# Optimization experiments

Measured on AMD Instinct MI355X. Metric: run time of the kernel, lower is better.

## Reference

```python
import jax, jax.numpy as jnp
import numpy as np

D_MODEL = 1024
NUM_HEADS = 16


def setup_inputs() -> dict:
    key = jax.random.key(0)
    ks = jax.random.split(key, 5)
    std = 1.0 / np.sqrt(D_MODEL)
    def w(k):
        return jnp.clip(jax.random.normal(k, (D_MODEL, D_MODEL), dtype=jnp.float32) * std, -3.0, 3.0)
    return {
        "x": jax.random.normal(ks[0], (4, 2048, D_MODEL), dtype=jnp.float32),
        "Wq": w(ks[1]),
        "Wk": w(ks[2]),
        "Wv": w(ks[3]),
        "Wo": w(ks[4]),
    }


def _mha(x, Wq, Wk, Wv, Wo):
    B, S, D = x.shape
    H = NUM_HEADS
    hd = D // H
    # Linear: y = x @ W.T (weights stored [d_out, d_in])
    def proj(W):
        y = jnp.einsum('bsd,ed->bse', x, W)
        return y.reshape(B, S, H, hd).transpose(0, 2, 1, 3)  # b h s d
    q, k, v = proj(Wq), proj(Wk), proj(Wv)
    scores = jnp.einsum('bhqd,bhkd->bhqk', q, k) / np.sqrt(hd)
    causal = jnp.tril(jnp.ones((S, S), dtype=bool))
    scores = jnp.where(causal, scores, -jnp.inf)
    attn = jax.nn.softmax(scores, axis=-1)
    a = jnp.einsum('bhqk,bhkd->bhqd', attn, v)
    a = a.transpose(0, 2, 1, 3).reshape(B, S, D)
    return jnp.einsum('bsd,ed->bse', a, Wo)


def reference(x, Wq, Wk, Wv, Wo):
    return _mha(x, Wq, Wk, Wv, Wo)
```

## Files before the change

kernel.cpp:

```cpp
#include <hip/hip_runtime.h>
#include <hip/hip_bf16.h>
#include <cstdint>
#include <cstddef>


typedef short bf16x8 __attribute__((ext_vector_type(8)));
typedef float f32x4 __attribute__((ext_vector_type(4)));
typedef unsigned int u32x2 __attribute__((ext_vector_type(2)));

__device__ __forceinline__ short f2bf(float f) {
    union { float f; uint32_t u; } c; c.f = f;
    uint32_t r = c.u + 0x7fffu + ((c.u >> 16) & 1u);
    return (short)(r >> 16);
}

__device__ __forceinline__ unsigned cvt_pk_bf16(float lo, float hi) {
    unsigned r;
    asm("v_cvt_pk_bf16_f32 %0, %1, %2" : "=v"(r) : "v"(lo), "v"(hi));
    return r;
}

#define GLOAD_LDS16(g, l) __builtin_amdgcn_global_load_lds( \
    (const __attribute__((address_space(1))) void*)(g),     \
    (__attribute__((address_space(3))) void*)(l), 16, 0, 0)

__global__ __launch_bounds__(256) void convert_kernel(const float* __restrict__ src,
                                                      short* __restrict__ dst) {
    int i = blockIdx.x * 256 + threadIdx.x;
    const float4* s = (const float4*)src + (size_t)i * 2;
    float4 v0 = s[0], v1 = s[1];
    bf16x8 o;
    o[0] = f2bf(v0.x); o[1] = f2bf(v0.y); o[2] = f2bf(v0.z); o[3] = f2bf(v0.w);
    o[4] = f2bf(v1.x); o[5] = f2bf(v1.y); o[6] = f2bf(v1.z); o[7] = f2bf(v1.w);
    *((bf16x8*)dst + i) = o;
}

__global__ __launch_bounds__(256) void convert_w4(const float* __restrict__ w0,
                                                  const float* __restrict__ w1,
                                                  const float* __restrict__ w2,
                                                  const float* __restrict__ w3,
                                                  short* __restrict__ dst) {
    int id = blockIdx.x;
    const float* s = (id < 512) ? w0 : (id < 1024) ? w1 : (id < 1536) ? w2 : w3;
    int i = (id & 511) * 256 + threadIdx.x;
    const float4* sp = (const float4*)s + (size_t)i * 2;
    float4 v0 = sp[0], v1 = sp[1];
    bf16x8 o;
    o[0] = f2bf(v0.x); o[1] = f2bf(v0.y); o[2] = f2bf(v0.z); o[3] = f2bf(v0.w);
    o[4] = f2bf(v1.x); o[5] = f2bf(v1.y); o[6] = f2bf(v1.z); o[7] = f2bf(v1.w);
    *((bf16x8*)(dst + (size_t)(id >> 9) * 1024 * 1024) + i) = o;
}

template<bool OUT_F32>
__device__ __forceinline__ void gemm_body(const short* __restrict__ A,
                                          const short* __restrict__ Bw,
                                          void* __restrict__ Outp,
                                          float escale) {
    __shared__ short As[128 * 32];
    __shared__ short Bs[128 * 32];
    const int tid = threadIdx.x;
    const int lane = tid & 63, w = tid >> 6;
    const int wr = w >> 1, wc = w & 1;
    const int l15 = lane & 15, l4 = lane >> 4;
    const int lin = blockIdx.y * 8 + blockIdx.x;
    const int eff = (lin & 7) * 64 + (lin >> 3);
    const size_t m0 = (size_t)(eff >> 3) * 128;
    const size_t n0 = (size_t)(eff & 7) * 128;

    f32x4 acc[4][4];
    const f32x4 zf = {0.f, 0.f, 0.f, 0.f};
    #pragma unroll
    for (int i = 0; i < 4; i++)
        #pragma unroll
        for (int j = 0; j < 4; j++) acc[i][j] = zf;

    for (int k0 = 0; k0 < 1024; k0 += 32) {
        #pragma unroll
        for (int r = 0; r < 2; r++) {
            int c = r * 256 + tid;
            int row = c >> 2, q = c & 3;
            GLOAD_LDS16(A  + (m0 + row) * 1024 + k0 + q * 8, &As[(r * 256 + w * 64) * 8]);
            GLOAD_LDS16(Bw + (n0 + row) * 1024 + k0 + q * 8, &Bs[(r * 256 + w * 64) * 8]);
        }
        __syncthreads();

        bf16x8 af[4], bfr[4];
        #pragma unroll
        for (int mi = 0; mi < 4; mi++)
            af[mi] = *(const bf16x8*)&As[(wr * 64 + mi * 16 + l15) * 32 + l4 * 8];
        #pragma unroll
        for (int ni = 0; ni < 4; ni++)
            bfr[ni] = *(const bf16x8*)&Bs[(wc * 64 + ni * 16 + l15) * 32 + l4 * 8];
        #pragma unroll
        for (int mi = 0; mi < 4; mi++)
            #pragma unroll
            for (int ni = 0; ni < 4; ni++)
                acc[mi][ni] = __builtin_amdgcn_mfma_f32_16x16x32_bf16(af[mi], bfr[ni], acc[mi][ni], 0, 0, 0);
        __syncthreads();
    }

    #pragma unroll
    for (int mi = 0; mi < 4; mi++) {
        #pragma unroll
        for (int ni = 0; ni < 4; ni++) {
            size_t row = m0 + wr * 64 + mi * 16 + (l4 << 2);
            size_t col = n0 + wc * 64 + ni * 16 + l15;
            #pragma unroll
            for (int j = 0; j < 4; j++) {
                float v = acc[mi][ni][j] * escale;
                if (OUT_F32) ((float*)Outp)[(row + j) * 1024 + col] = v;
                else         ((short*)Outp)[(row + j) * 1024 + col] = f2bf(v);
            }
        }
    }
}

__global__ __launch_bounds__(256) void gemm_qkv(const short* __restrict__ xb,
                                                const short* __restrict__ Wq,
                                                const short* __restrict__ Wk,
                                                const short* __restrict__ Wv,
                                                short* __restrict__ Q,
                                                short* __restrict__ K,
                                                short* __restrict__ V) {
    const short* Bw = (blockIdx.z == 0) ? Wq : (blockIdx.z == 1) ? Wk : Wv;
    short* Out      = (blockIdx.z == 0) ? Q  : (blockIdx.z == 1) ? K  : V;
    float sc = (blockIdx.z == 0) ? 0.18033688011112042f : 1.0f;
    gemm_body<false>(xb, Bw, Out, sc);
}

__global__ __launch_bounds__(256) void gemm_out(const short* __restrict__ Aw,
                                                const short* __restrict__ Wo,
                                                float* __restrict__ Out) {
    gemm_body<true>(Aw, Wo, Out, 1.0f);
}

__global__ __launch_bounds__(256) void transpose_v(const short* __restrict__ Vw,
                                                   short* __restrict__ Vt) {
    __shared__ short T[64][72];
    const int tid = threadIdx.x;
    const int s0 = blockIdx.x * 64;
    const int bh = blockIdx.y, b = bh >> 4, h = bh & 15;
    const int r = tid >> 2, c = tid & 3;
    const size_t srow = (size_t)(b * 2048 + s0 + r) * 1024 + h * 64 + c * 16;
    *(bf16x8*)&T[r][c * 16]     = *(const bf16x8*)&Vw[srow];
    *(bf16x8*)&T[r][c * 16 + 8] = *(const bf16x8*)&Vw[srow + 8];
    __syncthreads();
    short tmp[16];
    #pragma unroll
    for (int i = 0; i < 16; i++) tmp[i] = T[c * 16 + i][r];
    bf16x8 o0, o1;
    #pragma unroll
    for (int i = 0; i < 8; i++) { o0[i] = tmp[i]; o1[i] = tmp[8 + i]; }
    size_t orow = (size_t)(bh * 64 + r) * 2048 + s0 + c * 16;
    *(bf16x8*)&Vt[orow] = o0;
    *(bf16x8*)&Vt[orow + 8] = o1;
}

__global__ __launch_bounds__(512, 4) void attn_kernel(const short* __restrict__ Q,
                                                      const short* __restrict__ K,
                                                      const short* __restrict__ Vt,
                                                      short* __restrict__ Aout) {
    __shared__ __align__(16) short K_lds[2][64 * 64];
    __shared__ __align__(16) short V_lds[2][64 * 64];
    __shared__ __align__(16) short P_lds[8][16][72];
    const int tid = threadIdx.x;
    const int lane = tid & 63, w = tid >> 6;
    const int l15 = lane & 15, l4 = lane >> 4;
    const int bh = blockIdx.x, b = bh >> 4, h = bh & 15;
    const int y = blockIdx.y;
    const int qblk = (y < 4) ? (7 - y) : (y - 4);
    const int qw0 = qblk * 256 + w * 32;
    const short* Qg = Q + (size_t)b * 2048 * 1024 + h * 64;
    const short* Kg = K + (size_t)b * 2048 * 1024 + h * 64;
    const short* Vg = Vt + (size_t)bh * 64 * 2048;

    const int srow = (lane >> 3);
    const int scol = ((lane & 7) ^ srow) * 8;

    bf16x8 qfr[2][2];
    #pragma unroll
    for (int qf = 0; qf < 2; qf++)
        #pragma unroll
        for (int ks = 0; ks < 2; ks++)
            qfr[qf][ks] = *(const bf16x8*)&Qg[(size_t)(qw0 + qf * 16 + l15) * 1024 + ks * 32 + l4 * 8];

    const f32x4 zf = {0.f, 0.f, 0.f, 0.f};
    f32x4 oacc[4][2];
    float l_s[2] = {0.f, 0.f};
    #pragma unroll
    for (int df = 0; df < 4; df++)
        #pragma unroll
        for (int qf = 0; qf < 2; qf++) oacc[df][qf] = zf;

    const int lim = 4 * qblk + 3;

#define KV_RD(base, r, cb) (*(const bf16x8*)((const char*)(base) + (r) * 128 + ((cb) ^ (((r) & 7) << 4))))

    GLOAD_LDS16(Kg + (size_t)(w * 8 + srow) * 1024 + scol, &K_lds[0][w * 512]);
    GLOAD_LDS16(Vg + (size_t)(w * 8 + srow) * 2048 + scol, &V_lds[0][w * 512]);
    __syncthreads();

    int buf = 0;
    for (int t = 0; t <= lim; ++t) {
        const int kv0 = t * 64;
        if (t < lim) {
            const int nv0 = kv0 + 64;
            GLOAD_LDS16(Kg + (size_t)(nv0 + w * 8 + srow) * 1024 + scol, &K_lds[buf ^ 1][w * 512]);
            GLOAD_LDS16(Vg + (size_t)(w * 8 + srow) * 2048 + nv0 + scol, &V_lds[buf ^ 1][w * 512]);
        }

        const int lim_w = (qw0 + 31) >> 6;
        if (t <= lim_w) {
            const short* Kb = K_lds[buf];
            const short* Vb = V_lds[buf];

            f32x4 sacc[4][2];
            #pragma unroll
            for (int kvf = 0; kvf < 4; kvf++)
                #pragma unroll
                for (int qf = 0; qf < 2; qf++) sacc[kvf][qf] = zf;
            __builtin_amdgcn_s_setprio(1);
            #pragma unroll
            for (int kvf = 0; kvf < 4; kvf++) {
                bf16x8 kf0 = KV_RD(Kb, kvf * 16 + l15, l4 * 16);
                bf16x8 kf1 = KV_RD(Kb, kvf * 16 + l15, 64 + l4 * 16);
                #pragma unroll
                for (int qf = 0; qf < 2; qf++) {
                    sacc[kvf][qf] = __builtin_amdgcn_mfma_f32_16x16x32_bf16(kf0, qfr[qf][0], sacc[kvf][qf], 0, 0, 0);
                    sacc[kvf][qf] = __builtin_amdgcn_mfma_f32_16x16x32_bf16(kf1, qfr[qf][1], sacc[kvf][qf], 0, 0, 0);
                }
            }
            __builtin_amdgcn_s_setprio(0);

            if (t == lim_w) {
                #pragma unroll
                for (int kvf = 0; kvf < 4; kvf++)
                    #pragma unroll
                    for (int qf = 0; qf < 2; qf++)
                        #pragma unroll
                        for (int j = 0; j < 4; j++) {
                            int kvg = kv0 + kvf * 16 + l4 * 4 + j;
                            int qg  = qw0 + qf * 16 + l15;
                            if (kvg > qg) sacc[kvf][qf][j] = -1e30f;
                        }
            }

            #pragma unroll
            for (int qf = 0; qf < 2; qf++) {
                float rk[4];
                #pragma unroll
                for (int kvf = 0; kvf < 4; kvf++) {
                    float p0 = __builtin_amdgcn_exp2f(sacc[kvf][qf][0]);
                    float p1 = __builtin_amdgcn_exp2f(sacc[kvf][qf][1]);
                    float p2 = __builtin_amdgcn_exp2f(sacc[kvf][qf][2]);
                    float p3 = __builtin_amdgcn_exp2f(sacc[kvf][qf][3]);
                    sacc[kvf][qf][0] = p0; sacc[kvf][qf][1] = p1;
                    sacc[kvf][qf][2] = p2; sacc[kvf][qf][3] = p3;
                    rk[kvf] = (p0 + p1) + (p2 + p3);
                }
                l_s[qf] += (rk[0] + rk[1]) + (rk[2] + rk[3]);
                #pragma unroll
                for (int kvf = 0; kvf < 4; kvf++) {
                    u32x2 pr;
                    pr[0] = cvt_pk_bf16(sacc[kvf][qf][0], sacc[kvf][qf][1]);
                    pr[1] = cvt_pk_bf16(sacc[kvf][qf][2], sacc[kvf][qf][3]);
                    *(u32x2*)&P_lds[w][l15][kvf * 16 + l4 * 4] = pr;
                }
                asm volatile("s_waitcnt lgkmcnt(0)" ::: "memory");
                __builtin_amdgcn_sched_barrier(0);

                bf16x8 pf0 = *(const bf16x8*)&P_lds[w][l15][l4 * 8];
                bf16x8 pf1 = *(const bf16x8*)&P_lds[w][l15][32 + l4 * 8];

                __builtin_amdgcn_s_setprio(1);
                #pragma unroll
                for (int df = 0; df < 4; df++) {
                    bf16x8 v0 = KV_RD(Vb, df * 16 + l15, l4 * 16);
                    bf16x8 v1 = KV_RD(Vb, df * 16 + l15, 64 + l4 * 16);
                    oacc[df][qf] = __builtin_amdgcn_mfma_f32_16x16x32_bf16(v0, pf0, oacc[df][qf], 0, 0, 0);
                    oacc[df][qf] = __builtin_amdgcn_mfma_f32_16x16x32_bf16(v1, pf1, oacc[df][qf], 0, 0, 0);
                }
                __builtin_amdgcn_s_setprio(0);
            }
        }
        __syncthreads();
        buf ^= 1;
    }

    float rl[2];
    #pragma unroll
    for (int qf = 0; qf < 2; qf++) {
        float l = l_s[qf];
        l += __shfl_xor(l, 16);
        l += __shfl_xor(l, 32);
        rl[qf] = 1.f / l;
    }
    #pragma unroll
    for (int qf = 0; qf < 2; qf++) {
        #pragma unroll
        for (int df = 0; df < 4; df++) {
            u32x2 pr;
            pr[0] = cvt_pk_bf16(oacc[df][qf][0] * rl[qf], oacc[df][qf][1] * rl[qf]);
            pr[1] = cvt_pk_bf16(oacc[df][qf][2] * rl[qf], oacc[df][qf][3] * rl[qf]);
            *(u32x2*)&P_lds[w][l15][df * 16 + l4 * 4] = pr;
        }
        asm volatile("s_waitcnt lgkmcnt(0)" ::: "memory");
        __builtin_amdgcn_sched_barrier(0);
        const int r = lane >> 2, cq = lane & 3;
        size_t orow = (size_t)(b * 2048 + qw0 + qf * 16 + r) * 1024 + h * 64;
        *(bf16x8*)&Aout[orow + cq * 8]       = *(const bf16x8*)&P_lds[w][r][cq * 8];
        *(bf16x8*)&Aout[orow + (cq + 4) * 8] = *(const bf16x8*)&P_lds[w][r][(cq + 4) * 8];
        asm volatile("s_waitcnt lgkmcnt(0)" ::: "memory");
        __builtin_amdgcn_sched_barrier(0);
    }
#undef KV_RD
}

extern "C" void kernel_launch(void* const* d_in, const int* in_sizes, int n_in,
                              void* d_out, int out_size, void* d_ws, size_t ws_size,
                              hipStream_t stream) {
    const float* x  = (const float*)d_in[0];
    const float* Wq = (const float*)d_in[1];
    const float* Wk = (const float*)d_in[2];
    const float* Wv = (const float*)d_in[3];
    const float* Wo = (const float*)d_in[4];
    float* out = (float*)d_out;

    const size_t NX = (size_t)8192 * 1024;
    const size_t NW = (size_t)1024 * 1024;
    short* xb  = (short*)d_ws;
    short* Wqb = xb  + NX;
    short* Wkb = Wqb + NW;
    short* Wvb = Wkb + NW;
    short* Wob = Wvb + NW;
    short* Qw  = Wob + NW;
    short* Kw  = Qw + NX;
    short* Vw  = (short*)d_out;
    short* Vt  = Vw + NX;
    short* Aw  = xb;

    hipLaunchKernelGGL(convert_kernel, dim3(NX / 2048), dim3(256), 0, stream, x, xb);
    hipLaunchKernelGGL(convert_w4, dim3(2048), dim3(256), 0, stream, Wq, Wk, Wv, Wo, Wqb);

    hipLaunchKernelGGL(gemm_qkv, dim3(8, 64, 3), dim3(256), 0, stream, xb, Wqb, Wkb, Wvb, Qw, Kw, Vw);
    hipLaunchKernelGGL(transpose_v, dim3(32, 64), dim3(256), 0, stream, Vw, Vt);
    hipLaunchKernelGGL(attn_kernel, dim3(64, 8), dim3(512), 0, stream, Qw, Kw, Vt, Aw);
    hipLaunchKernelGGL(gemm_out, dim3(8, 64), dim3(256), 0, stream, Aw, Wob, out);
}
```

Before: 170.3 us.

## Double-buffer GEMM LDS tiles with K=64 and XOR-swizzled layout

New measurement: 168.9 us. Within noise of the previous version (-0.9%).

```diff
diff --git a/kernel.cpp b/kernel.cpp
--- a/kernel.cpp
+++ b/kernel.cpp
@@ -23,6 +23,8 @@
 #define GLOAD_LDS16(g, l) __builtin_amdgcn_global_load_lds( \
     (const __attribute__((address_space(1))) void*)(g),     \
     (__attribute__((address_space(3))) void*)(l), 16, 0, 0)
+
+#define SWZ_RD(base, r, cb) (*(const bf16x8*)((const char*)(base) + (size_t)(r) * 128 + ((cb) ^ (((r) & 7) << 4))))
 
 __global__ __launch_bounds__(256) void convert_kernel(const float* __restrict__ src,
                                                       short* __restrict__ dst) {
@@ -56,8 +58,8 @@
                                           const short* __restrict__ Bw,
                                           void* __restrict__ Outp,
                                           float escale) {
-    __shared__ short As[128 * 32];
-    __shared__ short Bs[128 * 32];
+    __shared__ __align__(16) short As[2][128 * 64];
+    __shared__ __align__(16) short Bs[2][128 * 64];
     const int tid = threadIdx.x;
     const int lane = tid & 63, w = tid >> 6;
     const int wr = w >> 1, wc = w & 1;
@@ -67,6 +69,22 @@
     const size_t m0 = (size_t)(eff >> 3) * 128;
     const size_t n0 = (size_t)(eff & 7) * 128;
 
+    int srow[4], scol[4];
+    #pragma unroll
+    for (int i = 0; i < 4; i++) {
+        int c = i * 256 + tid;
+        srow[i] = c >> 3;
+        scol[i] = ((c & 7) ^ (srow[i] & 7)) * 8;
+    }
+
+    auto STAGE = [&](int bsel, int k0) {
+        #pragma unroll
+        for (int i = 0; i < 4; i++) {
+            GLOAD_LDS16(A  + (m0 + srow[i]) * 1024 + k0 + scol[i], &As[bsel][(i * 256 + w * 64) * 8]);
+            GLOAD_LDS16(Bw + (n0 + srow[i]) * 1024 + k0 + scol[i], &Bs[bsel][(i * 256 + w * 64) * 8]);
+        }
+    };
+
     f32x4 acc[4][4];
     const f32x4 zf = {0.f, 0.f, 0.f, 0.f};
     #pragma unroll
@@ -74,29 +92,37 @@
         #pragma unroll
         for (int j = 0; j < 4; j++) acc[i][j] = zf;
 
-    for (int k0 = 0; k0 < 1024; k0 += 32) {
-        #pragma unroll
-        for (int r = 0; r < 2; r++) {
-            int c = r * 256 + tid;
-            int row = c >> 2, q = c & 3;
-            GLOAD_LDS16(A  + (m0 + row) * 1024 + k0 + q * 8, &As[(r * 256 + w * 64) * 8]);
-            GLOAD_LDS16(Bw + (n0 + row) * 1024 + k0 + q * 8, &Bs[(r * 256 + w * 64) * 8]);
-        }
+    STAGE(0, 0);
+    __syncthreads();
+
+    int buf = 0;
+    for (int kt = 0; kt < 16; ++kt) {
+        if (kt < 15) STAGE(buf ^ 1, (kt + 1) * 64);
+
+        const short* Ab = As[buf];
+        const short* Bb = Bs[buf];
+        bf16x8 af[4][2], bfr[4][2];
+        #pragma unroll
+        for (int mi = 0; mi < 4; mi++) {
+            int r = wr * 64 + mi * 16 + l15;
+            af[mi][0] = SWZ_RD(Ab, r, l4 * 16);
+            af[mi][1] = SWZ_RD(Ab, r, 64 + l4 * 16);
+        }
+        #pragma unroll
+        for (int ni = 0; ni < 4; ni++) {
+            int r = wc * 64 + ni * 16 + l15;
+            bfr[ni][0] = SWZ_RD(Bb, r, l4 * 16);
+            bfr[ni][1] = SWZ_RD(Bb, r, 64 + l4 * 16);
+        }
+        #pragma unroll
+        for (int mi = 0; mi < 4; mi++)
+            #pragma unroll
+            for (int ni = 0; ni < 4; ni++) {
+                acc[mi][ni] = __builtin_amdgcn_mfma_f32_16x16x32_bf16(af[mi][0], bfr[ni][0], acc[mi][ni], 0, 0, 0);
+                acc[mi][ni] = __builtin_amdgcn_mfma_f32_16x16x32_bf16(af[mi][1], bfr[ni][1], acc[mi][ni], 0, 0, 0);
+            }
         __syncthreads();
-
-        bf16x8 af[4], bfr[4];
-        #pragma unroll
-        for (int mi = 0; mi < 4; mi++)
-            af[mi] = *(const bf16x8*)&As[(wr * 64 + mi * 16 + l15) * 32 + l4 * 8];
-        #pragma unroll
-        for (int ni = 0; ni < 4; ni++)
-            bfr[ni] = *(const bf16x8*)&Bs[(wc * 64 + ni * 16 + l15) * 32 + l4 * 8];
-        #pragma unroll
-        for (int mi = 0; mi < 4; mi++)
-            #pragma unroll
-            for (int ni = 0; ni < 4; ni++)
-                acc[mi][ni] = __builtin_amdgcn_mfma_f32_16x16x32_bf16(af[mi], bfr[ni], acc[mi][ni], 0, 0, 0);
-        __syncthreads();
+        buf ^= 1;
     }
 
     #pragma unroll
```

## Enlarge GEMM tile to 256x128 with double-buffered swizzled LDS staging

Applied to the files above, without the earlier changes.

After: 218.3 us. 1.28x slower.

```diff
diff --git a/kernel.cpp b/kernel.cpp
--- a/kernel.cpp
+++ b/kernel.cpp
@@ -23,6 +23,9 @@
 #define GLOAD_LDS16(g, l) __builtin_amdgcn_global_load_lds( \
     (const __attribute__((address_space(1))) void*)(g),     \
     (__attribute__((address_space(3))) void*)(l), 16, 0, 0)
+
+#define SWZ32_RD(base, r, cb) (*(const bf16x8*)((const char*)(base) + (size_t)(r) * 64 + ((cb) ^ (((r) & 3) << 4))))
+#define KV_RD(base, r, cb) (*(const bf16x8*)((const char*)(base) + (r) * 128 + ((cb) ^ (((r) & 7) << 4))))
 
 __global__ __launch_bounds__(256) void convert_kernel(const float* __restrict__ src,
                                                       short* __restrict__ dst) {
@@ -56,55 +59,77 @@
                                           const short* __restrict__ Bw,
                                           void* __restrict__ Outp,
                                           float escale) {
-    __shared__ short As[128 * 32];
-    __shared__ short Bs[128 * 32];
+    __shared__ __align__(16) short As[2][256 * 32];
+    __shared__ __align__(16) short Bs[2][128 * 32];
     const int tid = threadIdx.x;
     const int lane = tid & 63, w = tid >> 6;
-    const int wr = w >> 1, wc = w & 1;
     const int l15 = lane & 15, l4 = lane >> 4;
     const int lin = blockIdx.y * 8 + blockIdx.x;
-    const int eff = (lin & 7) * 64 + (lin >> 3);
-    const size_t m0 = (size_t)(eff >> 3) * 128;
+    const int eff = (lin & 7) * 32 + (lin >> 3);
+    const size_t m0 = (size_t)(eff >> 3) * 256;
     const size_t n0 = (size_t)(eff & 7) * 128;
 
-    f32x4 acc[4][4];
+    int rA[4], cA[4], rB[2], cB[2];
+    #pragma unroll
+    for (int i = 0; i < 4; i++) {
+        int c = i * 256 + tid;
+        rA[i] = c >> 2;
+        cA[i] = ((c & 3) ^ (rA[i] & 3)) * 8;
+    }
+    #pragma unroll
+    for (int i = 0; i < 2; i++) {
+        int c = i * 256 + tid;
+        rB[i] = c >> 2;
+        cB[i] = ((c & 3) ^ (rB[i] & 3)) * 8;
+    }
+
+    auto STAGE = [&](int bsel, int k0) {
+        #pragma unroll
+        for (int i = 0; i < 4; i++)
+            GLOAD_LDS16(A + (m0 + rA[i]) * 1024 + k0 + cA[i], &As[bsel][(i * 256 + (w << 6)) * 8]);
+        #pragma unroll
+        for (int i = 0; i < 2; i++)
+            GLOAD_LDS16(Bw + (n0 + rB[i]) * 1024 + k0 + cB[i], &Bs[bsel][(i * 256 + (w << 6)) * 8]);
+    };
+
+    f32x4 acc[4][8];
     const f32x4 zf = {0.f, 0.f, 0.f, 0.f};
     #pragma unroll
     for (int i = 0; i < 4; i++)
         #pragma unroll
-        for (int j = 0; j < 4; j++) acc[i][j] = zf;
-
-    for (int k0 = 0; k0 < 1024; k0 += 32) {
-        #pragma unroll
-        for (int r = 0; r < 2; r++) {
-            int c = r * 256 + tid;
-            int row = c >> 2, q = c & 3;
-            GLOAD_LDS16(A  + (m0 + row) * 1024 + k0 + q * 8, &As[(r * 256 + w * 64) * 8]);
-            GLOAD_LDS16(Bw + (n0 + row) * 1024 + k0 + q * 8, &Bs[(r * 256 + w * 64) * 8]);
-        }
-        __syncthreads();
-
-        bf16x8 af[4], bfr[4];
+        for (int j = 0; j < 8; j++) acc[i][j] = zf;
+
+    STAGE(0, 0);
+    __syncthreads();
+
+    int buf = 0;
+    for (int kt = 0; kt < 32; ++kt) {
+        if (kt < 31) STAGE(buf ^ 1, (kt + 1) * 32);
+
+        const short* Ab = As[buf];
+        const short* Bb = Bs[buf];
+        bf16x8 af[4], bfr[8];
         #pragma unroll
         for (int mi = 0; mi < 4; mi++)
-            af[mi] = *(const bf16x8*)&As[(wr * 64 + mi * 16 + l15) * 32 + l4 * 8];
-        #pragma unroll
-        for (int ni = 0; ni < 4; ni++)
-            bfr[ni] = *(const bf16x8*)&Bs[(wc * 64 + ni * 16 + l15) * 32 + l4 * 8];
+            af[mi] = SWZ32_RD(Ab, (w << 6) + mi * 16 + l15, l4 * 16);
+        #pragma unroll
+        for (int ni = 0; ni < 8; ni++)
+            bfr[ni] = SWZ32_RD(Bb, ni * 16 + l15, l4 * 16);
         #pragma unroll
         for (int mi = 0; mi < 4; mi++)
             #pragma unroll
-            for (int ni = 0; ni < 4; ni++)
+            for (int ni = 0; ni < 8; ni++)
                 acc[mi][ni] = __builtin_amdgcn_mfma_f32_16x16x32_bf16(af[mi], bfr[ni], acc[mi][ni], 0, 0, 0);
         __syncthreads();
+        buf ^= 1;
     }
 
     #pragma unroll
     for (int mi = 0; mi < 4; mi++) {
         #pragma unroll
-        for (int ni = 0; ni < 4; ni++) {
-            size_t row = m0 + wr * 64 + mi * 16 + (l4 << 2);
-            size_t col = n0 + wc * 64 + ni * 16 + l15;
+        for (int ni = 0; ni < 8; ni++) {
+            size_t row = m0 + (w << 6) + mi * 16 + (l4 << 2);
+            size_t col = n0 + ni * 16 + l15;
             #pragma unroll
             for (int j = 0; j < 4; j++) {
                 float v = acc[mi][ni][j] * escale;
@@ -194,8 +219,6 @@
 
     const int lim = 4 * qblk + 3;
 
-#define KV_RD(base, r, cb) (*(const bf16x8*)((const char*)(base) + (r) * 128 + ((cb) ^ (((r) & 7) << 4))))
-
     GLOAD_LDS16(Kg + (size_t)(w * 8 + srow) * 1024 + scol, &K_lds[0][w * 512]);
     GLOAD_LDS16(Vg + (size_t)(w * 8 + srow) * 2048 + scol, &V_lds[0][w * 512]);
     __syncthreads();
@@ -313,7 +336,6 @@
         asm volatile("s_waitcnt lgkmcnt(0)" ::: "memory");
         __builtin_amdgcn_sched_barrier(0);
     }
-#undef KV_RD
 }
 
 extern "C" void kernel_launch(void* const* d_in, const int* in_sizes, int n_in,
@@ -342,8 +364,8 @@
     hipLaunchKernelGGL(convert_kernel, dim3(NX / 2048), dim3(256), 0, stream, x, xb);
     hipLaunchKernelGGL(convert_w4, dim3(2048), dim3(256), 0, stream, Wq, Wk, Wv, Wo, Wqb);
 
-    hipLaunchKernelGGL(gemm_qkv, dim3(8, 64, 3), dim3(256), 0, stream, xb, Wqb, Wkb, Wvb, Qw, Kw, Vw);
+    hipLaunchKernelGGL(gemm_qkv, dim3(8, 32, 3), dim3(256), 0, stream, xb, Wqb, Wkb, Wvb, Qw, Kw, Vw);
     hipLaunchKernelGGL(transpose_v, dim3(32, 64), dim3(256), 0, stream, Vw, Vt);
     hipLaunchKernelGGL(attn_kernel, dim3(64, 8), dim3(512), 0, stream, Qw, Kw, Vt, Aw);
-    hipLaunchKernelGGL(gemm_out, dim3(8, 64), dim3(256), 0, stream, Aw, Wob, out);
-}
+    hipLaunchKernelGGL(gemm_out, dim3(8, 32), dim3(256), 0, stream, Aw, Wob, out);
+}
```
